# Performance work log

Measured on AMD Instinct MI355X. Metric: run time of the kernel, lower is better.

## Reference

```python
import jax, jax.numpy as jnp
import numpy as np

N = 50000


def cheb_conv(x, row, col, deg_inv_sqrt, diag_w, W, b):
    """PyG ChebConv with K=3, normalization='sym', lambda_max=2.
    L~ = 2L/lambda_max - I = -D^{-1/2} A D^{-1/2} (diag 0 for deg>0, -1 for isolated).
    T0 = x, T1 = L~ x, T2 = 2 L~ T1 - T0; out = sum_k Tk @ W[k] + b.
    """
    w = -deg_inv_sqrt[row] * deg_inv_sqrt[col]  # [E]

    def Lhat(h):
        # message: w_e * h[src], aggregated at dst (source_to_target flow)
        agg = jax.ops.segment_sum(w[:, None] * h[col], row, num_segments=N)
        return agg + diag_w[:, None] * h

    Tx0 = x
    Tx1 = Lhat(x)
    Tx2 = 2.0 * Lhat(Tx1) - Tx0
    return Tx0 @ W[0] + Tx1 @ W[1] + Tx2 @ W[2] + b


def setup_inputs() -> dict:
    key = jax.random.key(0)
    ks = jax.random.split(key, 8)
    x = jax.random.normal(ks[0], (N, 512), dtype=jnp.float32)
    edge_index = jax.random.randint(ks[1], (2, 1600000), 0, N, dtype=jnp.int64)
    w1 = jax.random.normal(ks[2], (3, 512, 250), dtype=jnp.float32) * 0.05
    b1 = jnp.zeros((250,), dtype=jnp.float32)
    w2 = jax.random.normal(ks[3], (3, 250, 500), dtype=jnp.float32) * 0.05
    b2 = jnp.zeros((500,), dtype=jnp.float32)
    w3 = jax.random.normal(ks[4], (3, 500, 1000), dtype=jnp.float32) * 0.05
    b3 = jnp.zeros((1000,), dtype=jnp.float32)
    return {"x": x, "edge_index": edge_index, "w1": w1, "b1": b1,
            "w2": w2, "b2": b2, "w3": w3, "b3": b3}


def reference(x, edge_index, w1, b1, w2, b2, w3, b3):
    row, col = edge_index[1], edge_index[0]  # dst, src (source_to_target)
    # symmetric-normalization degree (computed as in PyG get_laplacian: scatter on row)
    deg = jax.ops.segment_sum(jnp.ones(edge_index.shape[1], dtype=x.dtype), row,
                              num_segments=N)
    deg_inv_sqrt = jnp.where(deg > 0, jax.lax.rsqrt(jnp.maximum(deg, 1.0)), 0.0)
    diag_w = jnp.where(deg > 0, 0.0, -1.0).astype(x.dtype)  # 2*L_ii/lmax - 1

    h = jax.nn.relu(cheb_conv(x, row, col, deg_inv_sqrt, diag_w, w1, b1))
    h = jax.nn.relu(cheb_conv(h, row, col, deg_inv_sqrt, diag_w, w2, b2))
    h = jax.nn.relu(cheb_conv(h, row, col, deg_inv_sqrt, diag_w, w3, b3))
    return h
```

## Files before the change

kernel.cpp:

```cpp
#include <hip/hip_runtime.h>


typedef unsigned short u16;
typedef __attribute__((ext_vector_type(8))) short s16x8;
typedef __attribute__((ext_vector_type(4))) float f32x4;
typedef __attribute__((ext_vector_type(8))) unsigned short u16x8;
typedef __attribute__((ext_vector_type(4))) unsigned short u16x4;

__device__ __forceinline__ float b2f(u16 u) {
  union { unsigned int i; float f; } x; x.i = ((unsigned int)u) << 16; return x.f;
}
__device__ __forceinline__ u16 f2b(float f) {
  union { float f; unsigned int i; } x; x.f = f;
  unsigned int r = x.i + 0x7fffu + ((x.i >> 16) & 1u);
  return (u16)(r >> 16);
}

typedef __attribute__((address_space(1))) unsigned int gu32_t;
typedef __attribute__((address_space(3))) unsigned int lu32_t;
__device__ __forceinline__ void gload16(const void* g, void* l) {
  __builtin_amdgcn_global_load_lds((const gu32_t*)g, (lu32_t*)l, 16, 0, 0);
}

__global__ void k_zero_i32(int* p, int n) {
  int t = blockIdx.x * 256 + threadIdx.x;
  if (t < n) p[t] = 0;
}

__global__ void k_hist(const int* __restrict__ ei, int* __restrict__ cnt, int E) {
  int e = blockIdx.x * 256 + threadIdx.x;
  if (e < E) atomicAdd(&cnt[ei[E + e]], 1);
}

__global__ void k_dis(const int* __restrict__ cnt, float* __restrict__ dis, int N) {
  int t = blockIdx.x * 256 + threadIdx.x;
  if (t < N) dis[t] = cnt[t] > 0 ? rsqrtf((float)cnt[t]) : 0.f;
}

__global__ void k_scan1(const int* __restrict__ cnt, int* __restrict__ part, int N) {
  __shared__ int s[256];
  int t = threadIdx.x, idx = blockIdx.x * 256 + t;
  s[t] = idx < N ? cnt[idx] : 0;
  __syncthreads();
  for (int o = 128; o > 0; o >>= 1) {
    if (t < o) s[t] += s[t + o];
    __syncthreads();
  }
  if (t == 0) part[blockIdx.x] = s[0];
}

__global__ void k_scan2(int* part, int nb, int* csroff, int N, int E) {
  if (threadIdx.x == 0 && blockIdx.x == 0) {
    int run = 0;
    for (int b = 0; b < nb; ++b) { int v = part[b]; part[b] = run; run += v; }
    csroff[N] = E;
  }
}

__global__ void k_scan3(const int* __restrict__ cnt, const int* __restrict__ part,
                        int* __restrict__ csroff, int* __restrict__ cursor, int N) {
  __shared__ int s[256];
  int t = threadIdx.x, idx = blockIdx.x * 256 + t;
  int v = idx < N ? cnt[idx] : 0;
  s[t] = v;
  __syncthreads();
  for (int o = 1; o < 256; o <<= 1) {
    int add = t >= o ? s[t - o] : 0;
    __syncthreads();
    s[t] += add;
    __syncthreads();
  }
  if (idx < N) {
    int ex = part[blockIdx.x] + s[t] - v;
    csroff[idx] = ex;
    cursor[idx] = ex;
  }
}

__global__ void k_scatter(const int* __restrict__ ei, int* __restrict__ cursor,
                          int* __restrict__ csrsrc, int E) {
  int e = blockIdx.x * 256 + threadIdx.x;
  if (e >= E) return;
  int s = ei[e];
  int d = ei[E + e];
  int pos = atomicAdd(&cursor[d], 1);
  csrsrc[pos] = s;
}

__global__ void k_convx(const float* __restrict__ x, u16* __restrict__ C, int N, int NPAD) {
  int t = blockIdx.x * 256 + threadIdx.x;
  int row = t >> 6;
  if (row >= NPAD) return;
  int c0 = (t & 63) * 8;
  u16x8 o;
  if (row < N) {
    const float4* p = (const float4*)(x + (size_t)row * 512 + c0);
    float4 a = p[0], b = p[1];
    o[0] = f2b(a.x); o[1] = f2b(a.y); o[2] = f2b(a.z); o[3] = f2b(a.w);
    o[4] = f2b(b.x); o[5] = f2b(b.y); o[6] = f2b(b.z); o[7] = f2b(b.w);
  } else {
#pragma unroll
    for (int j = 0; j < 8; ++j) o[j] = 0;
  }
  *(u16x8*)(C + (size_t)row * 512 + c0) = o;
}

__global__ void k_convw_kblk(const float* __restrict__ W, u16* __restrict__ Wb,
                             int Fin, int Kpad, int Nout) {
  int n = blockIdx.x;
  int ldw = 3 * Kpad;
  for (int kk = threadIdx.x; kk < ldw; kk += 256) {
    int ck = kk / Kpad, k = kk - ck * Kpad;
    float v = (k < Fin && n < Nout) ? W[((size_t)ck * Fin + k) * Nout + n] : 0.f;
    Wb[(size_t)n * ldw + kk] = f2b(v);
  }
}

__global__ void k_convw_nblk(const float* __restrict__ W, u16* __restrict__ Wb,
                             int Nout ) {
  int n = blockIdx.x;
  int ck = n >> 8, j = n & 255;
  for (int k = threadIdx.x; k < 512; k += 256) {
    float v = (j < Nout) ? W[((size_t)ck * 512 + k) * Nout + j] : 0.f;
    Wb[(size_t)n * 512 + k] = f2b(v);
  }
}

template <int FV> struct UV;
template <> struct UV<8> { using T = u16x8; };
template <> struct UV<4> { using T = u16x4; };

template <int FV, int MODE>
__global__ __launch_bounds__(256) void spmm_k(
    const u16* __restrict__ G, int ldg,
    const u16* __restrict__ E0, const u16* __restrict__ E1, int lde,
    const float* __restrict__ bias, int nreal,
    u16* __restrict__ O, int ldo,
    const int* __restrict__ off, const int* __restrict__ srcs,
    const float* __restrict__ dis, int N) {
  using uvec = typename UV<FV>::T;
  const int r = blockIdx.x * 4 + (threadIdx.x >> 6);
  if (r >= N) return;
  const int c0 = (threadIdx.x & 63) * FV;
  const u16* __restrict__ Gc = G + c0;
  float acc[FV];
#pragma unroll
  for (int j = 0; j < FV; ++j) acc[j] = 0.f;
  int e = off[r];
  const int e1 = off[r + 1];
  for (; e + 2 <= e1; e += 2) {
    const int s0 = srcs[e], s1 = srcs[e + 1];
    const float w0 = dis[s0], w1 = dis[s1];
    const uvec v0 = *(const uvec*)(Gc + (size_t)s0 * ldg);
    const uvec v1 = *(const uvec*)(Gc + (size_t)s1 * ldg);
#pragma unroll
    for (int j = 0; j < FV; ++j) acc[j] += w0 * b2f(v0[j]) + w1 * b2f(v1[j]);
  }
  if (e < e1) {
    const int s0 = srcs[e];
    const float w0 = dis[s0];
    const uvec v0 = *(const uvec*)(Gc + (size_t)s0 * ldg);
#pragma unroll
    for (int j = 0; j < FV; ++j) acc[j] += w0 * b2f(v0[j]);
  }
  const float disr = dis[r];
  float lap[FV];
#pragma unroll
  for (int j = 0; j < FV; ++j) lap[j] = -disr * acc[j];
  if (disr == 0.f) {
    const uvec v = *(const uvec*)(Gc + (size_t)r * ldg);
#pragma unroll
    for (int j = 0; j < FV; ++j) lap[j] -= b2f(v[j]);
  }
  uvec o;
  if constexpr (MODE == 0) {
#pragma unroll
    for (int j = 0; j < FV; ++j) o[j] = f2b(lap[j]);
  } else if constexpr (MODE == 1) {
    const uvec h = *(const uvec*)(E0 + (size_t)r * lde + c0);
#pragma unroll
    for (int j = 0; j < FV; ++j) o[j] = f2b(2.f * lap[j] - b2f(h[j]));
  } else if constexpr (MODE == 2) {
    const uvec u1 = *(const uvec*)(E0 + (size_t)r * lde + c0);
#pragma unroll
    for (int j = 0; j < FV; ++j) o[j] = f2b(b2f(u1[j]) + 2.f * lap[j]);
  } else {
    const uvec u0 = *(const uvec*)(E0 + (size_t)r * lde + c0);
    const uvec u2 = *(const uvec*)(E1 + (size_t)r * lde + c0);
#pragma unroll
    for (int j = 0; j < FV; ++j) {
      const int c = c0 + j;
      const float bv = (c < nreal) ? bias[c] : 0.f;
      float v = b2f(u0[j]) - b2f(u2[j]) + lap[j] + bv;
      o[j] = f2b(v > 0.f ? v : 0.f);
    }
  }
  *(uvec*)(O + (size_t)r * ldo + c0) = o;
}

template <typename OUTT, bool ACT>
__global__ __launch_bounds__(256) void gemm_k(
    const u16* __restrict__ A, int lda,
    const u16* __restrict__ B, int ldb,
    const float* __restrict__ bias,
    OUTT* __restrict__ C, int ldc,
    int K, int nmask, int nreal, int Nrows, int NT) {
  __shared__ u16 As[128 * 64];
  __shared__ u16 Bs[128 * 64];
  const int tid = threadIdx.x;
  const int w = tid >> 6, l = tid & 63;

  const int nwg = gridDim.x;
  const int q = nwg >> 3, r8 = nwg & 7;
  const int xcd = blockIdx.x & 7, idx = blockIdx.x >> 3;
  const int wg = (xcd < r8 ? xcd * (q + 1) : r8 * (q + 1) + (xcd - r8) * q) + idx;
  const int m0 = (wg / NT) * 128, n0 = (wg % NT) * 128;

  const int srow = w * 8 + (l >> 3);
  const int scol = ((l & 7) ^ (l >> 3)) * 8;
  const u16* ga = A + (size_t)m0 * lda + scol;
  const u16* gb = B + (size_t)n0 * ldb + scol;
  u16* lAs = &As[w * 512];
  u16* lBs = &Bs[w * 512];

  f32x4 acc[4][4];
#pragma unroll
  for (int m = 0; m < 4; ++m)
#pragma unroll
    for (int n = 0; n < 4; ++n) acc[m][n] = (f32x4){0.f, 0.f, 0.f, 0.f};

  const int wr = (w >> 1) * 64, wc = (w & 1) * 64;
  const int tr = l & 15, tg = l >> 4;
  const int rx = tr & 7;

  for (int k0 = 0; k0 < K; k0 += 64) {
    __syncthreads();
#pragma unroll
    for (int c = 0; c < 4; ++c) {
      gload16(ga + (size_t)(srow + c * 32) * lda + k0, lAs + c * 2048);
      gload16(gb + (size_t)(srow + c * 32) * ldb + k0, lBs + c * 2048);
    }
    __syncthreads();
#pragma unroll
    for (int kk = 0; kk < 64; kk += 32) {
      s16x8 af[4], bf[4];
#pragma unroll
      for (int m = 0; m < 4; ++m)
        af[m] = *(const s16x8*)&As[(wr + m * 16 + tr) * 64 + ((((kk >> 3) + tg) ^ rx) * 8)];
#pragma unroll
      for (int n = 0; n < 4; ++n)
        bf[n] = *(const s16x8*)&Bs[(wc + n * 16 + tr) * 64 + ((((kk >> 3) + tg) ^ rx) * 8)];
#pragma unroll
      for (int m = 0; m < 4; ++m)
#pragma unroll
        for (int n = 0; n < 4; ++n)
          acc[m][n] = __builtin_amdgcn_mfma_f32_16x16x32_bf16(af[m], bf[n], acc[m][n], 0, 0, 0);
    }
  }

#pragma unroll
  for (int m = 0; m < 4; ++m) {
    const int gr0 = m0 + wr + m * 16 + tg * 4;
#pragma unroll
    for (int n = 0; n < 4; ++n) {
      const int gc = n0 + wc + n * 16 + tr;
      const bool cv = (gc & nmask) < nreal;
      const float bv = (ACT && cv) ? bias[gc] : 0.f;
#pragma unroll
      for (int j = 0; j < 4; ++j) {
        float v = acc[m][n][j] + bv;
        if (ACT) v = v > 0.f ? v : 0.f;
        if constexpr (sizeof(OUTT) == 2) {
          C[(size_t)(gr0 + j) * ldc + gc] = cv ? f2b(v) : (u16)0;
        } else {
          if (gr0 + j < Nrows && cv)
            C[(size_t)(gr0 + j) * ldc + gc] = v;
        }
      }
    }
  }
}

extern "C" void kernel_launch(void* const* d_in, const int* in_sizes, int n_in,
                              void* d_out, int out_size, void* d_ws, size_t ws_size,
                              hipStream_t stream) {
  const float* x = (const float*)d_in[0];
  const int* ei = (const int*)d_in[1];
  const float* w1 = (const float*)d_in[2];
  const float* b1 = (const float*)d_in[3];
  const float* w2 = (const float*)d_in[4];
  const float* b2 = (const float*)d_in[5];
  const float* w3 = (const float*)d_in[6];
  const float* b3 = (const float*)d_in[7];
  float* out = (float*)d_out;

  const int N = in_sizes[0] / 512;
  const int E = in_sizes[1] / 2;
  const int NPAD = ((N + 127) / 128) * 128;
  const int NB = (N + 255) / 256;
  const int EB = (E + 255) / 256;
  const int MT = NPAD / 128;

  char* ws = (char*)d_ws;
  size_t o = 0;
  auto alloc = [&](size_t b) -> void* {
    void* p = ws + o;
    o = (o + b + 255) & ~(size_t)255;
    return p;
  };
  int* cnt = (int*)alloc((size_t)N * 4);
  float* dis = (float*)alloc((size_t)N * 4);
  int* csroff = (int*)alloc((size_t)(N + 1) * 4);
  int* cursor = (int*)alloc((size_t)N * 4);
  int* part = (int*)alloc(1024);
  int* csrsrc = (int*)alloc((size_t)E * 4);
  u16* CB = (u16*)alloc((size_t)NPAD * 768 * 2);
  u16* CA = (u16*)alloc((size_t)NPAD * 1536 * 2);
  u16* XB = CA;
  u16* U  = CA + (size_t)NPAD * 512;
  u16* P  = U  + (size_t)NPAD * 768;
  u16* Wb = (u16*)alloc((size_t)1024 * 1536 * 2);
  (void)ws_size; (void)n_in; (void)out_size;

  k_zero_i32<<<NB, 256, 0, stream>>>(cnt, N);
  k_hist<<<EB, 256, 0, stream>>>(ei, cnt, E);
  k_dis<<<NB, 256, 0, stream>>>(cnt, dis, N);
  k_scan1<<<NB, 256, 0, stream>>>(cnt, part, N);
  k_scan2<<<1, 64, 0, stream>>>(part, NB, csroff, N, E);
  k_scan3<<<NB, 256, 0, stream>>>(cnt, part, csroff, cursor, N);
  k_scatter<<<EB, 256, 0, stream>>>(ei, cursor, csrsrc, E);

  const int SG = (N + 3) / 4;

  k_convx<<<NPAD / 4, 256, 0, stream>>>(x, XB, N, NPAD);
  k_convw_nblk<<<768, 256, 0, stream>>>(w1, Wb, 250);
  gemm_k<u16, false><<<MT * 6, 256, 0, stream>>>(XB, 512, Wb, 512, nullptr,
                                                 U, 768, 512, 255, 250, N, 6);
  spmm_k<4, 2><<<SG, 256, 0, stream>>>(U + 512, 768, U + 256, (const u16*)nullptr, 768,
                                       nullptr, 0, P, 256, csroff, csrsrc, dis, N);
  spmm_k<4, 3><<<SG, 256, 0, stream>>>(P, 256, U, U + 512, 768,
                                       b1, 250, CB, 768, csroff, csrsrc, dis, N);

  k_convw_kblk<<<512, 256, 0, stream>>>(w2, Wb, 250, 256, 500);
  spmm_k<4, 0><<<SG, 256, 0, stream>>>(CB, 768, (const u16*)nullptr, (const u16*)nullptr, 0,
                                       nullptr, 0, CB + 256, 768, csroff, csrsrc, dis, N);
  spmm_k<4, 1><<<SG, 256, 0, stream>>>(CB + 256, 768, CB, (const u16*)nullptr, 768,
                                       nullptr, 0, CB + 512, 768, csroff, csrsrc, dis, N);
  gemm_k<u16, true><<<MT * 4, 256, 0, stream>>>(CB, 768, Wb, 768, b2,
                                                CA, 1536, 768, 511, 500, N, 4);

  k_convw_kblk<<<1024, 256, 0, stream>>>(w3, Wb, 500, 512, 1000);
  spmm_k<8, 0><<<SG, 256, 0, stream>>>(CA, 1536, (const u16*)nullptr, (const u16*)nullptr, 0,
                                       nullptr, 0, CA + 512, 1536, csroff, csrsrc, dis, N);
  spmm_k<8, 1><<<SG, 256, 0, stream>>>(CA + 512, 1536, CA, (const u16*)nullptr, 1536,
                                       nullptr, 0, CA + 1024, 1536, csroff, csrsrc, dis, N);
  gemm_k<float, true><<<MT * 8, 256, 0, stream>>>(CA, 1536, Wb, 1536, b3,
                                                  out, 1000, 1536, 1023, 1000, N, 8);
}
```

Measured before the change: 1.775 ms.

## Quantize SpMM gather operands to int8 with per-row scales

Before each sparse aggregation, a new kernel quantizes the bf16 feature rows to int8 with a per-row absmax scale, folded together with the degree normalization into a per-row weight. The SpMM then gathers int8 rows instead of bf16, halving the random-gather traffic, and the edge loop is unrolled by four. The cost is an extra quantization pass per SpMM and int8 precision loss in the propagated features. The output buffer is reused as scratch for the int8 copy.

```diff
diff --git a/kernel.cpp b/kernel.cpp
--- a/kernel.cpp
+++ b/kernel.cpp
@@ -6,6 +6,8 @@
 typedef __attribute__((ext_vector_type(4))) float f32x4;
 typedef __attribute__((ext_vector_type(8))) unsigned short u16x8;
 typedef __attribute__((ext_vector_type(4))) unsigned short u16x4;
+typedef __attribute__((ext_vector_type(8))) signed char s8x8;
+typedef __attribute__((ext_vector_type(4))) signed char s8x4;
 
 __device__ __forceinline__ float b2f(u16 u) {
   union { unsigned int i; float f; } x; x.i = ((unsigned int)u) << 16; return x.f;
@@ -126,51 +128,87 @@
   }
 }
 
-template <int FV> struct UV;
-template <> struct UV<8> { using T = u16x8; };
-template <> struct UV<4> { using T = u16x4; };
+template <int FV>
+__global__ __launch_bounds__(256) void k_quant(
+    const u16* __restrict__ T, int ldt, signed char* __restrict__ Q, int ldq,
+    const float* __restrict__ dis, float* __restrict__ qs, float* __restrict__ sc,
+    int N) {
+  using uvec = typename
+      __hip_internal::conditional<FV == 8, u16x8, u16x4>::type;
+  using qvec = typename
+      __hip_internal::conditional<FV == 8, s8x8, s8x4>::type;
+  const int r = blockIdx.x * 4 + (threadIdx.x >> 6);
+  if (r >= N) return;
+  const int l = threadIdx.x & 63, c0 = l * FV;
+  const uvec v = *(const uvec*)(T + (size_t)r * ldt + c0);
+  float f[FV];
+  float m = 0.f;
+#pragma unroll
+  for (int j = 0; j < FV; ++j) { f[j] = b2f(v[j]); m = fmaxf(m, fabsf(f[j])); }
+#pragma unroll
+  for (int o = 32; o > 0; o >>= 1) m = fmaxf(m, __shfl_xor(m, o, 64));
+  const float inv = m > 0.f ? 127.f / m : 0.f;
+  qvec q;
+#pragma unroll
+  for (int j = 0; j < FV; ++j) q[j] = (signed char)(int)rintf(f[j] * inv);
+  *(qvec*)(Q + (size_t)r * ldq + c0) = q;
+  if (l == 0) {
+    const float s = m > 0.f ? m * (1.f / 127.f) : 0.f;
+    sc[r] = s;
+    qs[r] = dis[r] * s;
+  }
+}
 
 template <int FV, int MODE>
-__global__ __launch_bounds__(256) void spmm_k(
-    const u16* __restrict__ G, int ldg,
+__global__ __launch_bounds__(256) void spmm_q(
+    const signed char* __restrict__ Q, int ldq,
+    const float* __restrict__ qs, const float* __restrict__ sc,
     const u16* __restrict__ E0, const u16* __restrict__ E1, int lde,
     const float* __restrict__ bias, int nreal,
     u16* __restrict__ O, int ldo,
     const int* __restrict__ off, const int* __restrict__ srcs,
     const float* __restrict__ dis, int N) {
-  using uvec = typename UV<FV>::T;
+  using uvec = typename
+      __hip_internal::conditional<FV == 8, u16x8, u16x4>::type;
+  using qvec = typename
+      __hip_internal::conditional<FV == 8, s8x8, s8x4>::type;
   const int r = blockIdx.x * 4 + (threadIdx.x >> 6);
   if (r >= N) return;
   const int c0 = (threadIdx.x & 63) * FV;
-  const u16* __restrict__ Gc = G + c0;
+  const signed char* __restrict__ Qc = Q + c0;
   float acc[FV];
 #pragma unroll
   for (int j = 0; j < FV; ++j) acc[j] = 0.f;
   int e = off[r];
   const int e1 = off[r + 1];
-  for (; e + 2 <= e1; e += 2) {
-    const int s0 = srcs[e], s1 = srcs[e + 1];
-    const float w0 = dis[s0], w1 = dis[s1];
-    const uvec v0 = *(const uvec*)(Gc + (size_t)s0 * ldg);
-    const uvec v1 = *(const uvec*)(Gc + (size_t)s1 * ldg);
-#pragma unroll
-    for (int j = 0; j < FV; ++j) acc[j] += w0 * b2f(v0[j]) + w1 * b2f(v1[j]);
-  }
-  if (e < e1) {
+  for (; e + 4 <= e1; e += 4) {
+    const int s0 = srcs[e], s1 = srcs[e + 1], s2 = srcs[e + 2], s3 = srcs[e + 3];
+    const float w0 = qs[s0], w1 = qs[s1], w2 = qs[s2], w3 = qs[s3];
+    const qvec v0 = *(const qvec*)(Qc + (size_t)s0 * ldq);
+    const qvec v1 = *(const qvec*)(Qc + (size_t)s1 * ldq);
+    const qvec v2 = *(const qvec*)(Qc + (size_t)s2 * ldq);
+    const qvec v3 = *(const qvec*)(Qc + (size_t)s3 * ldq);
+#pragma unroll
+    for (int j = 0; j < FV; ++j)
+      acc[j] += w0 * (float)v0[j] + w1 * (float)v1[j] +
+                w2 * (float)v2[j] + w3 * (float)v3[j];
+  }
+  for (; e < e1; ++e) {
     const int s0 = srcs[e];
-    const float w0 = dis[s0];
-    const uvec v0 = *(const uvec*)(Gc + (size_t)s0 * ldg);
-#pragma unroll
-    for (int j = 0; j < FV; ++j) acc[j] += w0 * b2f(v0[j]);
+    const float w0 = qs[s0];
+    const qvec v0 = *(const qvec*)(Qc + (size_t)s0 * ldq);
+#pragma unroll
+    for (int j = 0; j < FV; ++j) acc[j] += w0 * (float)v0[j];
   }
   const float disr = dis[r];
   float lap[FV];
 #pragma unroll
   for (int j = 0; j < FV; ++j) lap[j] = -disr * acc[j];
   if (disr == 0.f) {
-    const uvec v = *(const uvec*)(Gc + (size_t)r * ldg);
-#pragma unroll
-    for (int j = 0; j < FV; ++j) lap[j] -= b2f(v[j]);
+    const float s = sc[r];
+    const qvec v = *(const qvec*)(Qc + (size_t)r * ldq);
+#pragma unroll
+    for (int j = 0; j < FV; ++j) lap[j] -= s * (float)v[j];
   }
   uvec o;
   if constexpr (MODE == 0) {
@@ -313,6 +351,8 @@
   int* csroff = (int*)alloc((size_t)(N + 1) * 4);
   int* cursor = (int*)alloc((size_t)N * 4);
   int* part = (int*)alloc(1024);
+  float* qs = (float*)alloc((size_t)N * 4);
+  float* sc = (float*)alloc((size_t)N * 4);
   int* csrsrc = (int*)alloc((size_t)E * 4);
   u16* CB = (u16*)alloc((size_t)NPAD * 768 * 2);
   u16* CA = (u16*)alloc((size_t)NPAD * 1536 * 2);
@@ -320,6 +360,7 @@
   u16* U  = CA + (size_t)NPAD * 512;
   u16* P  = U  + (size_t)NPAD * 768;
   u16* Wb = (u16*)alloc((size_t)1024 * 1536 * 2);
+  signed char* Q8 = (signed char*)d_out;
   (void)ws_size; (void)n_in; (void)out_size;
 
   k_zero_i32<<<NB, 256, 0, stream>>>(cnt, N);
@@ -336,23 +377,29 @@
   k_convw_nblk<<<768, 256, 0, stream>>>(w1, Wb, 250);
   gemm_k<u16, false><<<MT * 6, 256, 0, stream>>>(XB, 512, Wb, 512, nullptr,
                                                  U, 768, 512, 255, 250, N, 6);
-  spmm_k<4, 2><<<SG, 256, 0, stream>>>(U + 512, 768, U + 256, (const u16*)nullptr, 768,
+  k_quant<4><<<SG, 256, 0, stream>>>(U + 512, 768, Q8, 256, dis, qs, sc, N);
+  spmm_q<4, 2><<<SG, 256, 0, stream>>>(Q8, 256, qs, sc, U + 256, (const u16*)nullptr, 768,
                                        nullptr, 0, P, 256, csroff, csrsrc, dis, N);
-  spmm_k<4, 3><<<SG, 256, 0, stream>>>(P, 256, U, U + 512, 768,
+  k_quant<4><<<SG, 256, 0, stream>>>(P, 256, Q8, 256, dis, qs, sc, N);
+  spmm_q<4, 3><<<SG, 256, 0, stream>>>(Q8, 256, qs, sc, U, U + 512, 768,
                                        b1, 250, CB, 768, csroff, csrsrc, dis, N);
 
   k_convw_kblk<<<512, 256, 0, stream>>>(w2, Wb, 250, 256, 500);
-  spmm_k<4, 0><<<SG, 256, 0, stream>>>(CB, 768, (const u16*)nullptr, (const u16*)nullptr, 0,
+  k_quant<4><<<SG, 256, 0, stream>>>(CB, 768, Q8, 256, dis, qs, sc, N);
+  spmm_q<4, 0><<<SG, 256, 0, stream>>>(Q8, 256, qs, sc, (const u16*)nullptr, (const u16*)nullptr, 0,
                                        nullptr, 0, CB + 256, 768, csroff, csrsrc, dis, N);
-  spmm_k<4, 1><<<SG, 256, 0, stream>>>(CB + 256, 768, CB, (const u16*)nullptr, 768,
+  k_quant<4><<<SG, 256, 0, stream>>>(CB + 256, 768, Q8, 256, dis, qs, sc, N);
+  spmm_q<4, 1><<<SG, 256, 0, stream>>>(Q8, 256, qs, sc, CB, (const u16*)nullptr, 768,
                                        nullptr, 0, CB + 512, 768, csroff, csrsrc, dis, N);
   gemm_k<u16, true><<<MT * 4, 256, 0, stream>>>(CB, 768, Wb, 768, b2,
                                                 CA, 1536, 768, 511, 500, N, 4);
 
   k_convw_kblk<<<1024, 256, 0, stream>>>(w3, Wb, 500, 512, 1000);
-  spmm_k<8, 0><<<SG, 256, 0, stream>>>(CA, 1536, (const u16*)nullptr, (const u16*)nullptr, 0,
+  k_quant<8><<<SG, 256, 0, stream>>>(CA, 1536, Q8, 512, dis, qs, sc, N);
+  spmm_q<8, 0><<<SG, 256, 0, stream>>>(Q8, 512, qs, sc, (const u16*)nullptr, (const u16*)nullptr, 0,
                                        nullptr, 0, CA + 512, 1536, csroff, csrsrc, dis, N);
-  spmm_k<8, 1><<<SG, 256, 0, stream>>>(CA + 512, 1536, CA, (const u16*)nullptr, 1536,
+  k_quant<8><<<SG, 256, 0, stream>>>(CA + 512, 1536, Q8, 512, dis, qs, sc, N);
+  spmm_q<8, 1><<<SG, 256, 0, stream>>>(Q8, 512, qs, sc, CA, (const u16*)nullptr, 1536,
                                        nullptr, 0, CA + 1024, 1536, csroff, csrsrc, dis, N);
   gemm_k<float, true><<<MT * 8, 256, 0, stream>>>(CA, 1536, Wb, 1536, b3,
                                                   out, 1000, 1536, 1023, 1000, N, 8);
```

Measured after the change: 1.443 ms. -18.7%, faster.
